# Performance work log

Measured on AMD Instinct MI355X. Metric: run time of the kernel, lower is better.

## Reference

```python
import jax, jax.numpy as jnp
import numpy as np

MOMENTUM = 0.1  # from init_kwargs


def setup_inputs() -> dict:
    key = jax.random.key(0)
    k1, k2 = jax.random.split(key)
    # [B, C, H, W] image batch
    x = jax.random.normal(k1, (32, 3, 512, 512), dtype=jnp.float32)
    # running amplitude buffer [C, H, W]; nonzero -> EMA branch is exercised
    running_amp = jax.random.uniform(k2, (3, 512, 512), dtype=jnp.float32)
    return {"x": x, "running_amp": running_amp}


def reference(x, running_amp):
    # FFT over spatial dims
    fft = jnp.fft.fft2(x, axes=(-2, -1))                     # [B,C,H,W] complex64
    amp = jnp.fft.fftshift(jnp.abs(fft), axes=(-2, -1))      # centered amplitude
    pha = jnp.angle(fft)                                     # phase

    # EMA update of running amplitude (batch-mean); if buffer is all-zero it is
    # initialized to the batch mean (mirrors the torch `sum == 0` branch).
    amp_mean = jnp.mean(amp, axis=0)                         # [C,H,W]
    new_amp = jnp.where(
        jnp.sum(running_amp) == 0,
        amp_mean,
        (1.0 - MOMENTUM) * running_amp + MOMENTUM * amp_mean,
    )

    # substitute amplitude with the (updated) running amplitude, keep phase
    amp_sub = jnp.fft.ifftshift(new_amp, axes=(-2, -1))      # [C,H,W]
    out = jnp.real(jnp.fft.ifft2(amp_sub * jnp.exp(1j * pha), axes=(-2, -1)))
    return out.astype(x.dtype)
```

## Files before the change

kernel.cpp:

```cpp
#include <hip/hip_runtime.h>
#include <hip/hip_fp16.h>
#include <math.h>

#define NB 32
#define NC 3
#define HH 512
#define WW 512
#define W2 272

typedef __half2 h2;
typedef unsigned long long ull;


__device__ __forceinline__ int swz(int i){ int h=(i>>6)&7; return i ^ (h<<3) ^ h; }
__device__ __forceinline__ int rev9(int k){ return ((k&7)<<6) | (k&56) | (k>>6); }

__device__ __forceinline__ float sin2pi(float x){
#if __has_builtin(__builtin_amdgcn_sinf)
  return __builtin_amdgcn_sinf(x);
#else
  return __sinf(6.28318530717958647692f*x);
#endif
}
__device__ __forceinline__ float cos2pi(float x){
#if __has_builtin(__builtin_amdgcn_cosf)
  return __builtin_amdgcn_cosf(x);
#else
  return __cosf(6.28318530717958647692f*x);
#endif
}

template<int S>
__device__ __forceinline__ void dft8(float* xr, float* xi){
  const float r2 = 0.70710678118654752f;
  float tr[4], ti[4], mr[4], mi[4];
#pragma unroll
  for(int n=0;n<4;n++){
    tr[n]=xr[n]+xr[n+4]; ti[n]=xi[n]+xi[n+4];
    mr[n]=xr[n]-xr[n+4]; mi[n]=xi[n]-xi[n+4];
  }
  float or_[4], oi_[4];
  or_[0]=mr[0];               oi_[0]=mi[0];
  or_[1]=r2*(mr[1]-S*mi[1]);  oi_[1]=r2*(mi[1]+S*mr[1]);
  or_[2]=-S*mi[2];            oi_[2]= S*mr[2];
  or_[3]=-r2*(mr[3]+S*mi[3]); oi_[3]= r2*(S*mr[3]-mi[3]);
  float s0r=tr[0]+tr[2], s0i=ti[0]+ti[2];
  float s1r=tr[1]+tr[3], s1i=ti[1]+ti[3];
  float d0r=tr[0]-tr[2], d0i=ti[0]-ti[2];
  float d1r=tr[1]-tr[3], d1i=ti[1]-ti[3];
  xr[0]=s0r+s1r;   xi[0]=s0i+s1i;
  xr[4]=s0r-s1r;   xi[4]=s0i-s1i;
  xr[2]=d0r-S*d1i; xi[2]=d0i+S*d1r;
  xr[6]=d0r+S*d1i; xi[6]=d0i-S*d1r;
  float p0r=or_[0]+or_[2], p0i=oi_[0]+oi_[2];
  float p1r=or_[1]+or_[3], p1i=oi_[1]+oi_[3];
  float e0r=or_[0]-or_[2], e0i=oi_[0]-oi_[2];
  float e1r=or_[1]-or_[3], e1i=oi_[1]-oi_[3];
  xr[1]=p0r+p1r;   xi[1]=p0i+p1i;
  xr[5]=p0r-p1r;   xi[5]=p0i-p1i;
  xr[3]=e0r-S*e1i; xi[3]=e0i+S*e1r;
  xr[7]=e0r+S*e1i; xi[7]=e0i-S*e1r;
}

template<int S>
__device__ __forceinline__ void twid(float* xr, float* xi, int n, float invM){
  float f = (float)n * invM;
  float c1 = cos2pi(f), s1 = (float)S * sin2pi(f);
  float cr=c1, ci=s1;
#pragma unroll
  for(int q=1;q<8;q++){
    float a=xr[q], b=xi[q];
    xr[q]=a*cr-b*ci; xi[q]=a*ci+b*cr;
    float nr=cr*c1-ci*s1, ni=cr*s1+ci*c1;
    cr=nr; ci=ni;
  }
}

__global__ __launch_bounds__(128) void k_row_rfft(const float* __restrict__ x, h2* __restrict__ Fh,
                                                  ull fh_cs){
  __shared__ float lre[2][512];
  __shared__ float lim[2][512];
  const int wv = threadIdx.x>>6, t = threadIdx.x&63;
  const int pr = blockIdx.x*2 + wv;
  const int b = pr>>8, r2 = pr&255;
  const int cc = blockIdx.y;
  const float* sa = x + (size_t)b*(NC*HH*WW) + (size_t)cc*HH*WW + (size_t)(2*r2)*WW;
  const float* sb = sa + WW;
  float xr[8], xi[8];
#pragma unroll
  for(int i=0;i<8;i++){ xr[i]=sa[t+64*i]; xi[i]=sb[t+64*i]; }
  dft8<-1>(xr,xi);
  twid<-1>(xr,xi,t,1.0f/512.0f);
#pragma unroll
  for(int q=0;q<8;q++){ int p=swz(t+64*q); lre[wv][p]=xr[q]; lim[wv][p]=xi[q]; }
  __syncthreads();
  const int beta=t>>3, n1=t&7, base1=64*beta+n1;
#pragma unroll
  for(int i=0;i<8;i++){ int p=swz(base1+8*i); xr[i]=lre[wv][p]; xi[i]=lim[wv][p]; }
  dft8<-1>(xr,xi);
  twid<-1>(xr,xi,n1,1.0f/64.0f);
#pragma unroll
  for(int q=0;q<8;q++){ int p=swz(base1+8*q); lre[wv][p]=xr[q]; lim[wv][p]=xi[q]; }
  __syncthreads();
#pragma unroll
  for(int i=0;i<8;i++){ int p=swz(8*t+i); xr[i]=lre[wv][p]; xi[i]=lim[wv][p]; }
  dft8<-1>(xr,xi);
  __syncthreads();
#pragma unroll
  for(int i=0;i<8;i++){ int nat = 64*i + 8*(t&7) + (t>>3); lre[wv][nat]=xr[i]; lim[wv][nat]=xi[i]; }
  __syncthreads();
  h2* Fa = Fh + (size_t)cc*fh_cs + (size_t)(b*HH + 2*r2)*W2;
  h2* Fb = Fa + W2;
#pragma unroll
  for(int j=0;j<5;j++){
    int w = t + 64*j;
    if(w<=256){
      int m = (512-w)&511;
      float pr_=lre[wv][w], pi_=lim[wv][w], qr=lre[wv][m], qi=lim[wv][m];
      Fa[w]=__float22half2_rn(make_float2(0.5f*(pr_+qr), 0.5f*(pi_-qi)));
      Fb[w]=__float22half2_rn(make_float2(0.5f*(pi_+qi), 0.5f*(qr-pr_)));
    }
  }
}

__global__ __launch_bounds__(512) void k_col_fft(h2* __restrict__ Fh, ull fh_cs,
                                                 float* __restrict__ Asum, ull a_cs){
  __shared__ float sre[512*17];
  __shared__ float sim[512*17];
  const int b    = blockIdx.x/17;
  const int tile = blockIdx.x - b*17;
  const int w0   = tile*16;
  const int cc   = blockIdx.y;
  h2*    base = Fh + (size_t)cc*fh_cs + (size_t)b*HH*W2 + w0;
  float* As   = Asum + (size_t)cc*a_cs + w0;
  const int c = threadIdx.x&15, w = threadIdx.x>>4;
#pragma unroll
  for(int jj=0;jj<2;jj++){
    int n = jj*32 + w;
    float xr[8], xi[8];
#pragma unroll
    for(int i=0;i<8;i++){ float2 v = __half22float2(base[(size_t)(n+64*i)*W2 + c]); xr[i]=v.x; xi[i]=v.y; }
    dft8<-1>(xr,xi);
    twid<-1>(xr,xi,n,1.0f/512.0f);
#pragma unroll
    for(int q=0;q<8;q++){ int e=n+64*q; sre[e*17+c]=xr[q]; sim[e*17+c]=xi[q]; }
  }
  __syncthreads();
#pragma unroll
  for(int jj=0;jj<2;jj++){
    int m = jj*32 + w;
    int bb = m>>3, nn = m&7, bs = 64*bb+nn;
    float xr[8], xi[8];
#pragma unroll
    for(int i=0;i<8;i++){ int e=bs+8*i; xr[i]=sre[e*17+c]; xi[i]=sim[e*17+c]; }
    dft8<-1>(xr,xi);
    twid<-1>(xr,xi,nn,1.0f/64.0f);
#pragma unroll
    for(int q=0;q<8;q++){ int e=bs+8*q; sre[e*17+c]=xr[q]; sim[e*17+c]=xi[q]; }
  }
  __syncthreads();
#pragma unroll
  for(int jj=0;jj<2;jj++){
    int m = jj*32+w;
    float xr[8], xi[8];
#pragma unroll
    for(int i=0;i<8;i++){ int e=8*m+i; xr[i]=sre[e*17+c]; xi[i]=sim[e*17+c]; }
    dft8<-1>(xr,xi);
    if(w0+c<=256){
#pragma unroll
      for(int q=0;q<8;q++){
        int p=8*m+q;
        base[(size_t)p*W2+c]=__float22half2_rn(make_float2(xr[q],xi[q]));
        atomicAdd(&As[(size_t)p*W2+c], sqrtf(xr[q]*xr[q]+xi[q]*xi[q]));
      }
    }
  }
}

__global__ __launch_bounds__(256) void k_rsum(const float* __restrict__ ra, float* __restrict__ out, int n){
  float s=0.f;
  for(int i=blockIdx.x*256+threadIdx.x; i<n; i+=gridDim.x*256) s+=ra[i];
#pragma unroll
  for(int off=32;off>=1;off>>=1) s += __shfl_down(s, off, 64);
  if((threadIdx.x&63)==0) atomicAdd(out, s);
}

__global__ __launch_bounds__(256) void k_amp_fin(const float* __restrict__ Asum, ull a_cs,
                                                 const float* __restrict__ ra, const float* __restrict__ rsum,
                                                 float* __restrict__ A){
  int f = blockIdx.x*256 + threadIdx.x;
  if(f >= HH*W2) return;
  int p = f/W2, w = f - p*W2;
  if(w>256) return;
  const int cc = blockIdx.y;
  float mean = Asum[(size_t)cc*a_cs + f]*(1.0f/32.0f);
  const float* rac = ra + (size_t)cc*HH*WW;
  int h = rev9(p);
  int hs =(h+256)&511, ws =(w+256)&511;
  int hs2=(256-h)&511, ws2=(256-w)&511;
  float a_ = (rsum[0]==0.0f) ? mean
           : 0.45f*(rac[hs*WW+ws] + rac[hs2*WW+ws2]) + 0.1f*mean;
  A[(size_t)cc*a_cs + f]=a_;
}

__global__ __launch_bounds__(512) void k_col_ifft(h2* __restrict__ Fh, ull fh_cs,
                                                  const float* __restrict__ A, ull a_cs){
  __shared__ float sre[512*17];
  __shared__ float sim[512*17];
  const int b    = blockIdx.x/17;
  const int tile = blockIdx.x - b*17;
  const int w0   = tile*16;
  const int cc   = blockIdx.y;
  h2* base = Fh + (size_t)cc*fh_cs + (size_t)b*HH*W2 + w0;
  const float* Aa = A + (size_t)cc*a_cs + w0;
  const int c = threadIdx.x&15, w = threadIdx.x>>4;
  const float invN2 = 1.0f/262144.0f;
#pragma unroll
  for(int jj=0;jj<2;jj++){
    int m = jj*32+w;
    float xr[8], xi[8];
#pragma unroll
    for(int q=0;q<8;q++){
      int p=8*m+q;
      float2 v = __half22float2(base[(size_t)p*W2+c]);
      float amp = Aa[(size_t)p*W2+c];
      float m2 = v.x*v.x + v.y*v.y;
      float sc = amp*invN2*__frsqrt_rn(m2);
      if(m2 > 0.f){ xr[q]=v.x*sc; xi[q]=v.y*sc; }
      else        { xr[q]=amp*invN2; xi[q]=0.f; }
    }
    dft8<1>(xr,xi);
#pragma unroll
    for(int i=0;i<8;i++){ int e=8*m+i; sre[e*17+c]=xr[i]; sim[e*17+c]=xi[i]; }
  }
  __syncthreads();
#pragma unroll
  for(int jj=0;jj<2;jj++){
    int m = jj*32 + w;
    int bb = m>>3, nn = m&7, bs = 64*bb+nn;
    float xr[8], xi[8];
#pragma unroll
    for(int q=0;q<8;q++){ int e=bs+8*q; xr[q]=sre[e*17+c]; xi[q]=sim[e*17+c]; }
    twid<1>(xr,xi,nn,1.0f/64.0f);
    dft8<1>(xr,xi);
#pragma unroll
    for(int i=0;i<8;i++){ int e=bs+8*i; sre[e*17+c]=xr[i]; sim[e*17+c]=xi[i]; }
  }
  __syncthreads();
#pragma unroll
  for(int jj=0;jj<2;jj++){
    int n = jj*32+w;
    float xr[8], xi[8];
#pragma unroll
    for(int q=0;q<8;q++){ int e=n+64*q; xr[q]=sre[e*17+c]; xi[q]=sim[e*17+c]; }
    twid<1>(xr,xi,n,1.0f/512.0f);
    dft8<1>(xr,xi);
    if(w0+c<=256){
#pragma unroll
      for(int i=0;i<8;i++){ base[(size_t)(n+64*i)*W2+c]=__float22half2_rn(make_float2(xr[i],xi[i])); }
    }
  }
}

__global__ __launch_bounds__(128) void k_row_irfft(const h2* __restrict__ Fh, ull fh_cs,
                                                   float* __restrict__ out){
  __shared__ h2 gA[2][264], gB[2][264];
  __shared__ float lre[2][512], lim[2][512];
  const int wv=threadIdx.x>>6, t=threadIdx.x&63;
  const int pr = blockIdx.x*2+wv;
  const int b = pr>>8, r2 = pr&255;
  const int cc = blockIdx.y;
  const h2* Rp = Fh + (size_t)cc*fh_cs + (size_t)(b*HH + 2*r2)*W2;
  const h2* Rq = Rp + W2;
#pragma unroll
  for(int j=0;j<5;j++){
    int w = t + 64*j;
    if(w<=256){ gA[wv][w]=Rp[w]; gB[wv][w]=Rq[w]; }
  }
  __syncthreads();
  float xr[8], xi[8];
#pragma unroll
  for(int i=0;i<8;i++){
    int w = rev9(8*t+i);
    float zr, zi;
    if(w<=256){
      float2 a = __half22float2(gA[wv][w]);
      float2 bb = __half22float2(gB[wv][w]);
      zr = a.x - bb.y; zi = a.y + bb.x;
    }else{
      int m = 512-w;
      float2 a = __half22float2(gA[wv][m]);
      float2 bb = __half22float2(gB[wv][m]);
      zr = a.x + bb.y; zi = bb.x - a.y;
    }
    xr[i]=zr; xi[i]=zi;
  }
  dft8<1>(xr,xi);
#pragma unroll
  for(int i=0;i<8;i++){ int pp=swz(8*t+i); lre[wv][pp]=xr[i]; lim[wv][pp]=xi[i]; }
  __syncthreads();
  const int beta=t>>3, n1=t&7, base1=64*beta+n1;
#pragma unroll
  for(int qq=0;qq<8;qq++){ int pp=swz(base1+8*qq); xr[qq]=lre[wv][pp]; xi[qq]=lim[wv][pp]; }
  twid<1>(xr,xi,n1,1.0f/64.0f);
  dft8<1>(xr,xi);
#pragma unroll
  for(int i=0;i<8;i++){ int pp=swz(base1+8*i); lre[wv][pp]=xr[i]; lim[wv][pp]=xi[i]; }
  __syncthreads();
#pragma unroll
  for(int qq=0;qq<8;qq++){ int pp=swz(t+64*qq); xr[qq]=lre[wv][pp]; xi[qq]=lim[wv][pp]; }
  twid<1>(xr,xi,t,1.0f/512.0f);
  dft8<1>(xr,xi);
  float* oa = out + (size_t)b*(NC*HH*WW) + (size_t)cc*HH*WW + (size_t)(2*r2)*WW;
  float* ob = oa + WW;
#pragma unroll
  for(int i=0;i<8;i++){ oa[t+64*i]=xr[i]; ob[t+64*i]=xi[i]; }
}

extern "C" void kernel_launch(void* const* d_in, const int* in_sizes, int n_in,
                              void* d_out, int out_size, void* d_ws, size_t ws_size,
                              hipStream_t stream) {
  const float* x  = (const float*)d_in[0];
  const float* ra = (const float*)d_in[1];
  float* out = (float*)d_out;

  const ull fh_cs = (ull)NB*HH*W2;
  const ull a_cs  = (ull)HH*W2;
  const size_t fb3 = (size_t)fh_cs*sizeof(h2)*3;
  const size_t ab1 = (size_t)a_cs*sizeof(float);
  const size_t need = fb3 + 3*ab1 + 64 + 3*ab1;
  if (ws_size < need) return;

  h2*    Fh   = (h2*)d_ws;
  float* Asum = (float*)((char*)d_ws + fb3);
  float* rsum = (float*)((char*)Asum + 3*ab1);
  float* A    = (float*)((char*)rsum + 64);

  hipMemsetAsync(Asum, 0, 3*ab1 + sizeof(float), stream);
  k_rsum<<<768,256,0,stream>>>(ra, rsum, NC*HH*WW);

  k_row_rfft <<<dim3(NB*256/2,3), 128, 0, stream>>>(x, Fh, fh_cs);
  k_col_fft  <<<dim3(NB*17,3),    512, 0, stream>>>(Fh, fh_cs, Asum, a_cs);
  k_amp_fin  <<<dim3((HH*W2+255)/256,3), 256, 0, stream>>>(Asum, a_cs, ra, rsum, A);
  k_col_ifft <<<dim3(NB*17,3),    512, 0, stream>>>(Fh, fh_cs, A, a_cs);
  k_row_irfft<<<dim3(NB*256/2,3), 128, 0, stream>>>(Fh, fh_cs, out);
}
```

Measured before the change: 198.8 us.

## Replace atomic amplitude sums with batch-reduction kernel and fp16 LDS staging

```diff
diff --git a/kernel.cpp b/kernel.cpp
--- a/kernel.cpp
+++ b/kernel.cpp
@@ -123,16 +123,13 @@
   }
 }
 
-__global__ __launch_bounds__(512) void k_col_fft(h2* __restrict__ Fh, ull fh_cs,
-                                                 float* __restrict__ Asum, ull a_cs){
-  __shared__ float sre[512*17];
-  __shared__ float sim[512*17];
+__global__ __launch_bounds__(512, 8) void k_col_fft(h2* __restrict__ Fh, ull fh_cs){
+  __shared__ h2 sld[512*17];
   const int b    = blockIdx.x/17;
   const int tile = blockIdx.x - b*17;
   const int w0   = tile*16;
   const int cc   = blockIdx.y;
-  h2*    base = Fh + (size_t)cc*fh_cs + (size_t)b*HH*W2 + w0;
-  float* As   = Asum + (size_t)cc*a_cs + w0;
+  h2* base = Fh + (size_t)cc*fh_cs + (size_t)b*HH*W2 + w0;
   const int c = threadIdx.x&15, w = threadIdx.x>>4;
 #pragma unroll
   for(int jj=0;jj<2;jj++){
@@ -143,7 +140,7 @@
     dft8<-1>(xr,xi);
     twid<-1>(xr,xi,n,1.0f/512.0f);
 #pragma unroll
-    for(int q=0;q<8;q++){ int e=n+64*q; sre[e*17+c]=xr[q]; sim[e*17+c]=xi[q]; }
+    for(int q=0;q<8;q++){ int e=n+64*q; sld[e*17+c]=__float22half2_rn(make_float2(xr[q],xi[q])); }
   }
   __syncthreads();
 #pragma unroll
@@ -152,11 +149,11 @@
     int bb = m>>3, nn = m&7, bs = 64*bb+nn;
     float xr[8], xi[8];
 #pragma unroll
-    for(int i=0;i<8;i++){ int e=bs+8*i; xr[i]=sre[e*17+c]; xi[i]=sim[e*17+c]; }
+    for(int i=0;i<8;i++){ int e=bs+8*i; float2 v=__half22float2(sld[e*17+c]); xr[i]=v.x; xi[i]=v.y; }
     dft8<-1>(xr,xi);
     twid<-1>(xr,xi,nn,1.0f/64.0f);
 #pragma unroll
-    for(int q=0;q<8;q++){ int e=bs+8*q; sre[e*17+c]=xr[q]; sim[e*17+c]=xi[q]; }
+    for(int q=0;q<8;q++){ int e=bs+8*q; sld[e*17+c]=__float22half2_rn(make_float2(xr[q],xi[q])); }
   }
   __syncthreads();
 #pragma unroll
@@ -164,14 +161,13 @@
     int m = jj*32+w;
     float xr[8], xi[8];
 #pragma unroll
-    for(int i=0;i<8;i++){ int e=8*m+i; xr[i]=sre[e*17+c]; xi[i]=sim[e*17+c]; }
+    for(int i=0;i<8;i++){ int e=8*m+i; float2 v=__half22float2(sld[e*17+c]); xr[i]=v.x; xi[i]=v.y; }
     dft8<-1>(xr,xi);
     if(w0+c<=256){
 #pragma unroll
       for(int q=0;q<8;q++){
         int p=8*m+q;
         base[(size_t)p*W2+c]=__float22half2_rn(make_float2(xr[q],xi[q]));
-        atomicAdd(&As[(size_t)p*W2+c], sqrtf(xr[q]*xr[q]+xi[q]*xi[q]));
       }
     }
   }
@@ -185,28 +181,41 @@
   if((threadIdx.x&63)==0) atomicAdd(out, s);
 }
 
-__global__ __launch_bounds__(256) void k_amp_fin(const float* __restrict__ Asum, ull a_cs,
-                                                 const float* __restrict__ ra, const float* __restrict__ rsum,
-                                                 float* __restrict__ A){
-  int f = blockIdx.x*256 + threadIdx.x;
-  if(f >= HH*W2) return;
-  int p = f/W2, w = f - p*W2;
-  if(w>256) return;
+__global__ __launch_bounds__(256) void k_amp(const h2* __restrict__ Fh, ull fh_cs,
+                                             const float* __restrict__ ra, const float* __restrict__ rsum,
+                                             float* __restrict__ A, ull a_cs){
+  int f2 = blockIdx.x*256 + threadIdx.x;
+  int p = f2/136, w2 = f2 - p*136;
+  int w = 2*w2;
   const int cc = blockIdx.y;
-  float mean = Asum[(size_t)cc*a_cs + f]*(1.0f/32.0f);
+  const float2* Fc = (const float2*)(Fh + (size_t)cc*fh_cs);
+  float s0=0.f, s1=0.f;
+#pragma unroll 8
+  for(int b=0;b<NB;b++){
+    float2 two = Fc[(size_t)b*(HH*W2/2) + f2];
+    h2 va = ((const h2*)&two)[0], vb = ((const h2*)&two)[1];
+    float2 a = __half22float2(va), bq = __half22float2(vb);
+    s0 += sqrtf(a.x*a.x + a.y*a.y);
+    s1 += sqrtf(bq.x*bq.x + bq.y*bq.y);
+  }
+  float mean0 = s0*(1.0f/32.0f), mean1 = s1*(1.0f/32.0f);
   const float* rac = ra + (size_t)cc*HH*WW;
   int h = rev9(p);
-  int hs =(h+256)&511, ws =(w+256)&511;
-  int hs2=(256-h)&511, ws2=(256-w)&511;
-  float a_ = (rsum[0]==0.0f) ? mean
-           : 0.45f*(rac[hs*WW+ws] + rac[hs2*WW+ws2]) + 0.1f*mean;
-  A[(size_t)cc*a_cs + f]=a_;
-}
-
-__global__ __launch_bounds__(512) void k_col_ifft(h2* __restrict__ Fh, ull fh_cs,
-                                                  const float* __restrict__ A, ull a_cs){
-  __shared__ float sre[512*17];
-  __shared__ float sim[512*17];
+  int hs =(h+256)&511, hs2=(256-h)&511;
+  int ws0 =(w+256)&511, ws20=(256-w)&511;
+  int ws1 =(w+257)&511, ws21=(255-w)&511;
+  float a0, a1;
+  if(rsum[0]==0.0f){ a0=mean0; a1=mean1; }
+  else{
+    a0 = 0.45f*(rac[hs*WW+ws0] + rac[hs2*WW+ws20]) + 0.1f*mean0;
+    a1 = 0.45f*(rac[hs*WW+ws1] + rac[hs2*WW+ws21]) + 0.1f*mean1;
+  }
+  *(float2*)(A + (size_t)cc*a_cs + (size_t)p*W2 + w) = make_float2(a0, a1);
+}
+
+__global__ __launch_bounds__(512, 8) void k_col_ifft(h2* __restrict__ Fh, ull fh_cs,
+                                                     const float* __restrict__ A, ull a_cs){
+  __shared__ h2 sld[512*17];
   const int b    = blockIdx.x/17;
   const int tile = blockIdx.x - b*17;
   const int w0   = tile*16;
@@ -231,7 +240,7 @@
     }
     dft8<1>(xr,xi);
 #pragma unroll
-    for(int i=0;i<8;i++){ int e=8*m+i; sre[e*17+c]=xr[i]; sim[e*17+c]=xi[i]; }
+    for(int i=0;i<8;i++){ int e=8*m+i; sld[e*17+c]=__float22half2_rn(make_float2(xr[i],xi[i])); }
   }
   __syncthreads();
 #pragma unroll
@@ -240,11 +249,11 @@
     int bb = m>>3, nn = m&7, bs = 64*bb+nn;
     float xr[8], xi[8];
 #pragma unroll
-    for(int q=0;q<8;q++){ int e=bs+8*q; xr[q]=sre[e*17+c]; xi[q]=sim[e*17+c]; }
+    for(int q=0;q<8;q++){ int e=bs+8*q; float2 v=__half22float2(sld[e*17+c]); xr[q]=v.x; xi[q]=v.y; }
     twid<1>(xr,xi,nn,1.0f/64.0f);
     dft8<1>(xr,xi);
 #pragma unroll
-    for(int i=0;i<8;i++){ int e=bs+8*i; sre[e*17+c]=xr[i]; sim[e*17+c]=xi[i]; }
+    for(int i=0;i<8;i++){ int e=bs+8*i; sld[e*17+c]=__float22half2_rn(make_float2(xr[i],xi[i])); }
   }
   __syncthreads();
 #pragma unroll
@@ -252,7 +261,7 @@
     int n = jj*32+w;
     float xr[8], xi[8];
 #pragma unroll
-    for(int q=0;q<8;q++){ int e=n+64*q; xr[q]=sre[e*17+c]; xi[q]=sim[e*17+c]; }
+    for(int q=0;q<8;q++){ int e=n+64*q; float2 v=__half22float2(sld[e*17+c]); xr[q]=v.x; xi[q]=v.y; }
     twid<1>(xr,xi,n,1.0f/512.0f);
     dft8<1>(xr,xi);
     if(w0+c<=256){
@@ -328,20 +337,19 @@
   const ull a_cs  = (ull)HH*W2;
   const size_t fb3 = (size_t)fh_cs*sizeof(h2)*3;
   const size_t ab1 = (size_t)a_cs*sizeof(float);
-  const size_t need = fb3 + 3*ab1 + 64 + 3*ab1;
+  const size_t need = fb3 + 64 + 3*ab1;
   if (ws_size < need) return;
 
   h2*    Fh   = (h2*)d_ws;
-  float* Asum = (float*)((char*)d_ws + fb3);
-  float* rsum = (float*)((char*)Asum + 3*ab1);
+  float* rsum = (float*)((char*)d_ws + fb3);
   float* A    = (float*)((char*)rsum + 64);
 
-  hipMemsetAsync(Asum, 0, 3*ab1 + sizeof(float), stream);
+  hipMemsetAsync(rsum, 0, sizeof(float), stream);
   k_rsum<<<768,256,0,stream>>>(ra, rsum, NC*HH*WW);
 
   k_row_rfft <<<dim3(NB*256/2,3), 128, 0, stream>>>(x, Fh, fh_cs);
-  k_col_fft  <<<dim3(NB*17,3),    512, 0, stream>>>(Fh, fh_cs, Asum, a_cs);
-  k_amp_fin  <<<dim3((HH*W2+255)/256,3), 256, 0, stream>>>(Asum, a_cs, ra, rsum, A);
+  k_col_fft  <<<dim3(NB*17,3),    512, 0, stream>>>(Fh, fh_cs);
+  k_amp      <<<dim3(HH*136/256,3),256, 0, stream>>>(Fh, fh_cs, ra, rsum, A, a_cs);
   k_col_ifft <<<dim3(NB*17,3),    512, 0, stream>>>(Fh, fh_cs, A, a_cs);
   k_row_irfft<<<dim3(NB*256/2,3), 128, 0, stream>>>(Fh, fh_cs, out);
 }
```

New measurement: 194.1 us (median of 2 runs). -2.4%, faster.
